# Kernel optimization log

Hardware: AMD Instinct MI355X
Metric: run time of the kernel (lower is better)

The kernel has to match this reference:

```python
import jax, jax.numpy as jnp
import numpy as np

R = 16
ALPHA = 32
SCALING = ALPHA / R  # 2.0
IN_F = 4096
OUT_F = 4096

def setup_inputs() -> dict:
    key = jax.random.key(0)
    k1, k2, k3, k4 = jax.random.split(key, 4)
    x = jax.random.normal(k1, (4, 2048, IN_F), dtype=jnp.float32)
    # kaiming_uniform init for lora_A in torch; randn is fine for a numeric baseline
    lora_A = jax.random.normal(k2, (R, IN_F), dtype=jnp.float32) * 0.02
    lora_B = jax.random.normal(k3, (OUT_F, R), dtype=jnp.float32) * 0.02
    bias = jax.random.normal(k4, (OUT_F,), dtype=jnp.float32) * 0.01
    return {"x": x, "lora_A": lora_A, "lora_B": lora_B, "bias": bias}

def reference(x, lora_A, lora_B, bias):
    # Faithful to torch: W = lora_B @ lora_A * scaling ([out, in]), then x @ W^T + bias
    W = (lora_B @ lora_A) * SCALING            # [out, in]
    out = jnp.einsum('bsi,oi->bso', x, W) + bias  # [B, S, out]
    return out
```

## Files before the change

kernel.cpp:

```cpp
#include <hip/hip_runtime.h>
#include <stdint.h>


constexpr int IN_F  = 4096;
constexpr int OUT_F = 4096;
constexpr int RANK  = 16;
constexpr int M_TOT = 4 * 2048;
constexpr float SCALING = 2.0f;

typedef const __attribute__((address_space(1))) void* as1_cvp;
typedef __attribute__((address_space(3))) void*       as3_vp;
typedef float f32x4 __attribute__((ext_vector_type(4)));

__global__ __launch_bounds__(512, 4) void lora_phase1(
    const float* __restrict__ x, const float* __restrict__ A,
    float* __restrict__ t)
{
    __shared__ float4 As[2][RANK][64];
    const int lane = threadIdx.x & 63;
    const int wave = threadIdx.x >> 6;
    const int row0 = blockIdx.x * 16 + wave * 2;

    const float4* __restrict__ A4 = (const float4*)A;
    const float4* __restrict__ x0 = (const float4*)(x + (size_t)row0 * IN_F);
    const float4* __restrict__ x1 = (const float4*)(x + (size_t)(row0 + 1) * IN_F);

    float acc0[RANK], acc1[RANK];
#pragma unroll
    for (int r = 0; r < RANK; ++r) { acc0[r] = 0.0f; acc1[r] = 0.0f; }

#pragma unroll
    for (int rr = 0; rr < 2; ++rr) {
        const int r = wave * 2 + rr;
        __builtin_amdgcn_global_load_lds((as1_cvp)(A4 + (size_t)r * (IN_F / 4) + lane),
                                         (as3_vp)(&As[0][r][0]), 16, 0, 0);
    }
    float4 xc0 = x0[lane];
    float4 xc1 = x1[lane];
    __syncthreads();

    int buf = 0;
#pragma unroll 1
    for (int j = 0; j < 16; ++j) {
        float4 xn0, xn1;
        if (j < 15) {
            const int c4 = (j + 1) * 64 + lane;
#pragma unroll
            for (int rr = 0; rr < 2; ++rr) {
                const int r = wave * 2 + rr;
                __builtin_amdgcn_global_load_lds(
                    (as1_cvp)(A4 + (size_t)r * (IN_F / 4) + c4),
                    (as3_vp)(&As[buf ^ 1][r][0]), 16, 0, 0);
            }
            xn0 = x0[c4];
            xn1 = x1[c4];
        }

#pragma unroll
        for (int r = 0; r < RANK; ++r) {
            const float4 av = As[buf][r][lane];
            acc0[r] += xc0.x * av.x;
            acc0[r] += xc0.y * av.y;
            acc0[r] += xc0.z * av.z;
            acc0[r] += xc0.w * av.w;
            acc1[r] += xc1.x * av.x;
            acc1[r] += xc1.y * av.y;
            acc1[r] += xc1.z * av.z;
            acc1[r] += xc1.w * av.w;
        }

        if (j < 15) {
            __syncthreads();
            buf ^= 1;
            xc0 = xn0;
            xc1 = xn1;
        }
    }

#pragma unroll
    for (int p = 0; p < 2; ++p) {
        float out_v = 0.0f;
#pragma unroll
        for (int r = 0; r < RANK; ++r) {
            float v = (p == 0) ? acc0[r] : acc1[r];
#pragma unroll
            for (int s = 1; s < 64; s <<= 1)
                v += __shfl_xor(v, s, 64);
            out_v = (lane == r) ? v : out_v;
        }
        if (lane < RANK)
            t[(size_t)(row0 + p) * RANK + lane] = SCALING * out_v;
    }
}

__global__ __launch_bounds__(256) void transpose_B(
    const float* __restrict__ B, float* __restrict__ BT)
{
    const int id = blockIdx.x * 256 + threadIdx.x;
    const float4 v = ((const float4*)B)[id];
    const int o = id >> 2;
    const int k = id & 3;
    BT[(size_t)(4 * k + 0) * OUT_F + o] = v.x;
    BT[(size_t)(4 * k + 1) * OUT_F + o] = v.y;
    BT[(size_t)(4 * k + 2) * OUT_F + o] = v.z;
    BT[(size_t)(4 * k + 3) * OUT_F + o] = v.w;
}

__global__ __launch_bounds__(256) void lora_phase2t(
    const float* __restrict__ t, const float* __restrict__ BT,
    const float* __restrict__ bias, float* __restrict__ out)
{
    const int o0 = blockIdx.x * 1024 + threadIdx.x * 4;
    const int m0 = blockIdx.y * 4;

    const f32x4* __restrict__ BT4 = (const f32x4*)BT;
    const float4* __restrict__ t4 = (const float4*)t;

    f32x4 b[16];
#pragma unroll
    for (int r = 0; r < 16; ++r)
        b[r] = BT4[(size_t)r * (OUT_F / 4) + (o0 >> 2)];

    float4 tv[4][4];
#pragma unroll
    for (int mi = 0; mi < 4; ++mi)
#pragma unroll
        for (int rr = 0; rr < 4; ++rr)
            tv[mi][rr] = t4[(size_t)(m0 + mi) * 4 + rr];

    const f32x4 bs = *(const f32x4*)(bias + o0);

#pragma unroll
    for (int mi = 0; mi < 4; ++mi) {
        f32x4 v = bs;
#pragma unroll
        for (int rr = 0; rr < 4; ++rr) {
            v += b[4 * rr + 0] * tv[mi][rr].x;
            v += b[4 * rr + 1] * tv[mi][rr].y;
            v += b[4 * rr + 2] * tv[mi][rr].z;
            v += b[4 * rr + 3] * tv[mi][rr].w;
        }
        *(f32x4*)(out + (size_t)(m0 + mi) * OUT_F + o0) = v;
    }
}

__global__ __launch_bounds__(256) void lora_phase2(
    const float* __restrict__ t, const float* __restrict__ B,
    const float* __restrict__ bias, float* __restrict__ out)
{
    const int o0 = blockIdx.x * 1024 + threadIdx.x * 4;
    const int m0 = blockIdx.y * 4;

    const float4* __restrict__ B4 = (const float4*)B;
    const float4* __restrict__ t4 = (const float4*)t;

    float4 b[4][4];
#pragma unroll
    for (int q = 0; q < 4; ++q)
#pragma unroll
        for (int rr = 0; rr < 4; ++rr)
            b[q][rr] = B4[(size_t)(o0 + q) * 4 + rr];

    float4 tv[4][4];
#pragma unroll
    for (int mi = 0; mi < 4; ++mi)
#pragma unroll
        for (int rr = 0; rr < 4; ++rr)
            tv[mi][rr] = t4[(size_t)(m0 + mi) * 4 + rr];

    const float4 bs = *(const float4*)(bias + o0);

#pragma unroll
    for (int mi = 0; mi < 4; ++mi) {
        float v[4] = {bs.x, bs.y, bs.z, bs.w};
#pragma unroll
        for (int q = 0; q < 4; ++q) {
#pragma unroll
            for (int rr = 0; rr < 4; ++rr) {
                v[q] += b[q][rr].x * tv[mi][rr].x;
                v[q] += b[q][rr].y * tv[mi][rr].y;
                v[q] += b[q][rr].z * tv[mi][rr].z;
                v[q] += b[q][rr].w * tv[mi][rr].w;
            }
        }
        float4 o4 = {v[0], v[1], v[2], v[3]};
        *(float4*)(out + (size_t)(m0 + mi) * OUT_F + o0) = o4;
    }
}

extern "C" void kernel_launch(void* const* d_in, const int* in_sizes, int n_in,
                              void* d_out, int out_size, void* d_ws, size_t ws_size,
                              hipStream_t stream) {
    const float* x    = (const float*)d_in[0];
    const float* A    = (const float*)d_in[1];
    const float* B    = (const float*)d_in[2];
    const float* bias = (const float*)d_in[3];
    float* out = (float*)d_out;
    float* t   = (float*)d_ws;

    const size_t need_bt = (size_t)(M_TOT * RANK + RANK * OUT_F) * sizeof(float);
    const bool use_bt = ws_size >= need_bt;
    float* BT = t + (size_t)M_TOT * RANK;

    if (use_bt)
        transpose_B<<<dim3(64), dim3(256), 0, stream>>>(B, BT);

    lora_phase1<<<dim3(M_TOT / 16), dim3(512), 0, stream>>>(x, A, t);

    if (use_bt)
        lora_phase2t<<<dim3(OUT_F / 1024, M_TOT / 4), dim3(256), 0, stream>>>(t, BT, bias, out);
    else
        lora_phase2<<<dim3(OUT_F / 1024, M_TOT / 4), dim3(256), 0, stream>>>(t, B, bias, out);
}
```

Measured before the change: 262.4 us.

## Fuse B transpose into phase1, raise rows per wave, enlarge phase2 M tile

Phase 1 now has each wave handle four rows instead of two, so each LDS read of A is reused across more rows. Launch bounds drop to 2 blocks per SM to make room for the extra accumulator registers. The separate transpose_B kernel is folded into the tail of the first 32 phase-1 blocks, removing one launch. Phase 2 processes 16 rows per block instead of 4, reusing the loaded B columns and bias over more outputs and cutting grid size. The risks are higher register pressure and lower occupancy in phase 1, plus uncoalesced B reads in the fused transpose.

```diff
diff --git a/kernel.cpp b/kernel.cpp
--- a/kernel.cpp
+++ b/kernel.cpp
@@ -5,29 +5,34 @@
 constexpr int IN_F  = 4096;
 constexpr int OUT_F = 4096;
 constexpr int RANK  = 16;
-constexpr int M_TOT = 4 * 2048;
+constexpr int M_TOT = 8192;
 constexpr float SCALING = 2.0f;
 
 typedef const __attribute__((address_space(1))) void* as1_cvp;
 typedef __attribute__((address_space(3))) void*       as3_vp;
 typedef float f32x4 __attribute__((ext_vector_type(4)));
 
-__global__ __launch_bounds__(512, 4) void lora_phase1(
+__global__ __launch_bounds__(512, 2) void lora_phase1(
     const float* __restrict__ x, const float* __restrict__ A,
-    float* __restrict__ t)
+    const float* __restrict__ B, float* __restrict__ t,
+    float* __restrict__ BT)
 {
     __shared__ float4 As[2][RANK][64];
     const int lane = threadIdx.x & 63;
     const int wave = threadIdx.x >> 6;
-    const int row0 = blockIdx.x * 16 + wave * 2;
+    const int row0 = blockIdx.x * 32 + wave * 4;
 
     const float4* __restrict__ A4 = (const float4*)A;
-    const float4* __restrict__ x0 = (const float4*)(x + (size_t)row0 * IN_F);
+    const float4* __restrict__ x0 = (const float4*)(x + (size_t)(row0 + 0) * IN_F);
     const float4* __restrict__ x1 = (const float4*)(x + (size_t)(row0 + 1) * IN_F);
-
-    float acc0[RANK], acc1[RANK];
-#pragma unroll
-    for (int r = 0; r < RANK; ++r) { acc0[r] = 0.0f; acc1[r] = 0.0f; }
+    const float4* __restrict__ x2 = (const float4*)(x + (size_t)(row0 + 2) * IN_F);
+    const float4* __restrict__ x3 = (const float4*)(x + (size_t)(row0 + 3) * IN_F);
+
+    float acc0[RANK], acc1[RANK], acc2[RANK], acc3[RANK];
+#pragma unroll
+    for (int r = 0; r < RANK; ++r) {
+        acc0[r] = 0.0f; acc1[r] = 0.0f; acc2[r] = 0.0f; acc3[r] = 0.0f;
+    }
 
 #pragma unroll
     for (int rr = 0; rr < 2; ++rr) {
@@ -37,12 +42,14 @@
     }
     float4 xc0 = x0[lane];
     float4 xc1 = x1[lane];
+    float4 xc2 = x2[lane];
+    float4 xc3 = x3[lane];
     __syncthreads();
 
     int buf = 0;
 #pragma unroll 1
     for (int j = 0; j < 16; ++j) {
-        float4 xn0, xn1;
+        float4 xn0, xn1, xn2, xn3;
         if (j < 15) {
             const int c4 = (j + 1) * 64 + lane;
 #pragma unroll
@@ -54,35 +61,37 @@
             }
             xn0 = x0[c4];
             xn1 = x1[c4];
+            xn2 = x2[c4];
+            xn3 = x3[c4];
         }
 
 #pragma unroll
         for (int r = 0; r < RANK; ++r) {
             const float4 av = As[buf][r][lane];
-            acc0[r] += xc0.x * av.x;
-            acc0[r] += xc0.y * av.y;
-            acc0[r] += xc0.z * av.z;
-            acc0[r] += xc0.w * av.w;
-            acc1[r] += xc1.x * av.x;
-            acc1[r] += xc1.y * av.y;
-            acc1[r] += xc1.z * av.z;
-            acc1[r] += xc1.w * av.w;
+            acc0[r] += xc0.x * av.x; acc0[r] += xc0.y * av.y;
+            acc0[r] += xc0.z * av.z; acc0[r] += xc0.w * av.w;
+            acc1[r] += xc1.x * av.x; acc1[r] += xc1.y * av.y;
+            acc1[r] += xc1.z * av.z; acc1[r] += xc1.w * av.w;
+            acc2[r] += xc2.x * av.x; acc2[r] += xc2.y * av.y;
+            acc2[r] += xc2.z * av.z; acc2[r] += xc2.w * av.w;
+            acc3[r] += xc3.x * av.x; acc3[r] += xc3.y * av.y;
+            acc3[r] += xc3.z * av.z; acc3[r] += xc3.w * av.w;
         }
 
         if (j < 15) {
             __syncthreads();
             buf ^= 1;
-            xc0 = xn0;
-            xc1 = xn1;
-        }
-    }
-
-#pragma unroll
-    for (int p = 0; p < 2; ++p) {
+            xc0 = xn0; xc1 = xn1; xc2 = xn2; xc3 = xn3;
+        }
+    }
+
+#pragma unroll
+    for (int p = 0; p < 4; ++p) {
         float out_v = 0.0f;
 #pragma unroll
         for (int r = 0; r < RANK; ++r) {
-            float v = (p == 0) ? acc0[r] : acc1[r];
+            float v = (p == 0) ? acc0[r] : (p == 1) ? acc1[r]
+                    : (p == 2) ? acc2[r] : acc3[r];
 #pragma unroll
             for (int s = 1; s < 64; s <<= 1)
                 v += __shfl_xor(v, s, 64);
@@ -91,19 +100,18 @@
         if (lane < RANK)
             t[(size_t)(row0 + p) * RANK + lane] = SCALING * out_v;
     }
-}
-
-__global__ __launch_bounds__(256) void transpose_B(
-    const float* __restrict__ B, float* __restrict__ BT)
-{
-    const int id = blockIdx.x * 256 + threadIdx.x;
-    const float4 v = ((const float4*)B)[id];
-    const int o = id >> 2;
-    const int k = id & 3;
-    BT[(size_t)(4 * k + 0) * OUT_F + o] = v.x;
-    BT[(size_t)(4 * k + 1) * OUT_F + o] = v.y;
-    BT[(size_t)(4 * k + 2) * OUT_F + o] = v.z;
-    BT[(size_t)(4 * k + 3) * OUT_F + o] = v.w;
+
+    if (BT != nullptr && blockIdx.x < 32) {
+        const int id = blockIdx.x * 512 + threadIdx.x;
+        const int r  = id >> 10;
+        const int c4 = id & 1023;
+        f32x4 v;
+        v.x = B[(size_t)(4 * c4 + 0) * RANK + r];
+        v.y = B[(size_t)(4 * c4 + 1) * RANK + r];
+        v.z = B[(size_t)(4 * c4 + 2) * RANK + r];
+        v.w = B[(size_t)(4 * c4 + 3) * RANK + r];
+        ((f32x4*)BT)[(size_t)r * (OUT_F / 4) + c4] = v;
+    }
 }
 
 __global__ __launch_bounds__(256) void lora_phase2t(
@@ -111,7 +119,7 @@
     const float* __restrict__ bias, float* __restrict__ out)
 {
     const int o0 = blockIdx.x * 1024 + threadIdx.x * 4;
-    const int m0 = blockIdx.y * 4;
+    const int m0 = blockIdx.y * 16;
 
     const f32x4* __restrict__ BT4 = (const f32x4*)BT;
     const float4* __restrict__ t4 = (const float4*)t;
@@ -121,25 +129,21 @@
     for (int r = 0; r < 16; ++r)
         b[r] = BT4[(size_t)r * (OUT_F / 4) + (o0 >> 2)];
 
-    float4 tv[4][4];
-#pragma unroll
-    for (int mi = 0; mi < 4; ++mi)
-#pragma unroll
-        for (int rr = 0; rr < 4; ++rr)
-            tv[mi][rr] = t4[(size_t)(m0 + mi) * 4 + rr];
-
     const f32x4 bs = *(const f32x4*)(bias + o0);
 
 #pragma unroll
-    for (int mi = 0; mi < 4; ++mi) {
+    for (int mi = 0; mi < 16; ++mi) {
+        const float4 tv0 = t4[(size_t)(m0 + mi) * 4 + 0];
+        const float4 tv1 = t4[(size_t)(m0 + mi) * 4 + 1];
+        const float4 tv2 = t4[(size_t)(m0 + mi) * 4 + 2];
+        const float4 tv3 = t4[(size_t)(m0 + mi) * 4 + 3];
+
         f32x4 v = bs;
-#pragma unroll
-        for (int rr = 0; rr < 4; ++rr) {
-            v += b[4 * rr + 0] * tv[mi][rr].x;
-            v += b[4 * rr + 1] * tv[mi][rr].y;
-            v += b[4 * rr + 2] * tv[mi][rr].z;
-            v += b[4 * rr + 3] * tv[mi][rr].w;
-        }
+        v += b[0]  * tv0.x; v += b[1]  * tv0.y; v += b[2]  * tv0.z; v += b[3]  * tv0.w;
+        v += b[4]  * tv1.x; v += b[5]  * tv1.y; v += b[6]  * tv1.z; v += b[7]  * tv1.w;
+        v += b[8]  * tv2.x; v += b[9]  * tv2.y; v += b[10] * tv2.z; v += b[11] * tv2.w;
+        v += b[12] * tv3.x; v += b[13] * tv3.y; v += b[14] * tv3.z; v += b[15] * tv3.w;
+
         *(f32x4*)(out + (size_t)(m0 + mi) * OUT_F + o0) = v;
     }
 }
@@ -202,13 +206,11 @@
     const bool use_bt = ws_size >= need_bt;
     float* BT = t + (size_t)M_TOT * RANK;
 
+    lora_phase1<<<dim3(M_TOT / 32), dim3(512), 0, stream>>>(
+        x, A, B, t, use_bt ? BT : nullptr);
+
     if (use_bt)
-        transpose_B<<<dim3(64), dim3(256), 0, stream>>>(B, BT);
-
-    lora_phase1<<<dim3(M_TOT / 16), dim3(512), 0, stream>>>(x, A, t);
-
-    if (use_bt)
-        lora_phase2t<<<dim3(OUT_F / 1024, M_TOT / 4), dim3(256), 0, stream>>>(t, BT, bias, out);
+        lora_phase2t<<<dim3(OUT_F / 1024, M_TOT / 16), dim3(256), 0, stream>>>(t, BT, bias, out);
     else
         lora_phase2<<<dim3(OUT_F / 1024, M_TOT / 4), dim3(256), 0, stream>>>(t, B, bias, out);
 }
```

After: 255.8 us. 2.5% less time.
